# Performance work log

Hardware: AMD Instinct MI355X
Metric: run time of the kernel (lower is better)

Reference implementation:

```python
import jax, jax.numpy as jnp
import numpy as np

P = 9  # patch_size


def setup_inputs() -> dict:
    key = jax.random.key(0)
    k1, k2, k3, k4 = jax.random.split(key, 4)
    B, Cin, D, H, W = 1, 128, 36, 72, 72
    Cout = 128
    L = (D // P) * ((H * W) // P)  # 2304 non-overlapping patches
    x = jax.random.normal(k1, (B, Cin, D, H, W), dtype=jnp.float32)
    attentions = jax.random.normal(k2, (B, Cout, L, P * P), dtype=jnp.float32)
    Wc = jax.random.normal(k3, (Cout, Cin), dtype=jnp.float32) * 0.05  # conv_img 1x1x1 weight
    b = jax.random.normal(k4, (Cout,), dtype=jnp.float32) * 0.05
    return {"x": x, "attentions": attentions, "W": Wc, "b": b}


def reference(x, attentions, W, b):
    # conv_img: 1x1x1 Conv3d == per-voxel channel GEMM
    y = jnp.einsum('oc,bcdhw->bodhw', W, x) + b[None, :, None, None, None]
    B, C, D, H, Wd = y.shape
    HW = H * Wd
    y2 = y.reshape(1, C, D, HW)  # [1, C, D, H*W] as in the torch reshape
    nD, nW = D // P, HW // P
    # Unfold with kernel=stride=P (non-overlapping) == block reshape.
    # Column order: patches row-major; row order: kernel positions row-major.
    patches = (y2.reshape(1, C, nD, P, nW, P)
                 .transpose(0, 1, 2, 4, 3, 5)
                 .reshape(1, C, nD * nW, P * P))  # [1, C, L, P*P]
    nz = jnp.count_nonzero(attentions, axis=-1).astype(y2.dtype)[..., None] + 1e-5
    att = patches + attentions / nz  # [1, C, L, P*P]
    # Fold (non-overlapping) == inverse block reshape; no overlap accumulation.
    corr = (att.reshape(1, C, nD, nW, P, P)
               .transpose(0, 1, 2, 4, 3, 5)
               .reshape(1, C, D, HW))
    out = corr * y2 + y2
    return jnp.where(out >= 0, out, 0.2 * out)  # LeakyReLU(0.2)
```

## Files before the change

kernel.cpp:

```cpp
#include <hip/hip_runtime.h>

#define CIN   128
#define COUT  128
#define DD    36
#define HW    5184
#define DHW   186624
#define PATCH 9
#define NPW   576
#define L_TOT 2304
#define PP    81
#define LDSK  136

typedef __attribute__((ext_vector_type(8))) short bf16x8;
typedef __attribute__((ext_vector_type(4))) float f32x4;

__device__ __forceinline__ short f2bf(float f) {
    unsigned u = __builtin_bit_cast(unsigned, f);
    unsigned r = (u + 0x7fffu + ((u >> 16) & 1u)) >> 16;
    return (short)r;
}
__device__ __forceinline__ float bf2f(short s) {
    return __builtin_bit_cast(float, ((unsigned)(unsigned short)s) << 16);
}

__global__ __launch_bounds__(256) void count_ballot(
    const float* __restrict__ attn, float* __restrict__ inv)
{
    const int wv   = threadIdx.x >> 6;
    const int lane = threadIdx.x & 63;
    const int w    = blockIdx.x * 4 + wv;

    const unsigned long long P0X = (1ull << 21) - 1;
    const unsigned long long P0Y = (1ull << 20) - 1;
    const unsigned long long P1X = ((1ull << 20) - 1) << 21;
    const unsigned long long P1Y = ((1ull << 21) - 1) << 20;
    const unsigned long long P1Z = ((1ull << 20) - 1) << 20;
    const unsigned long long P2X = ((1ull << 20) - 1) << 41;
    const unsigned long long P2Z = ((1ull << 21) - 1) << 40;
    const unsigned long long P2W = ((1ull << 20) - 1) << 40;
    const unsigned long long P3X = 0x7ull << 61;
    const unsigned long long P3W = 0xFull << 60;
    const unsigned long long TL  = (1ull << 17) - 1;

    #pragma unroll
    for (int k = 0; k < 4; ++k) {
        const int g = w * 4 + k;
        const float4* ap = (const float4*)attn + (size_t)g * 81;
        const float4 va = ap[lane];
        float4 vb = (float4){0.f, 0.f, 0.f, 0.f};
        if (lane < 17) vb = ap[64 + lane];

        const unsigned long long bx = __ballot(va.x != 0.f);
        const unsigned long long by = __ballot(va.y != 0.f);
        const unsigned long long bz = __ballot(va.z != 0.f);
        const unsigned long long bw = __ballot(va.w != 0.f);
        const unsigned long long tx = __ballot(vb.x != 0.f);
        const unsigned long long ty = __ballot(vb.y != 0.f);
        const unsigned long long tz = __ballot(vb.z != 0.f);
        const unsigned long long tw = __ballot(vb.w != 0.f);

        const int c0 = __popcll(bx & P0X) + __popcll(by & P0Y)
                     + __popcll(bz & P0Y) + __popcll(bw & P0Y);
        const int c1 = __popcll(bx & P1X) + __popcll(by & P1Y)
                     + __popcll(bz & P1Z) + __popcll(bw & P1Z);
        const int c2 = __popcll(bx & P2X) + __popcll(by & P2X)
                     + __popcll(bz & P2Z) + __popcll(bw & P2W);
        const int c3 = __popcll(bx & P3X) + __popcll(by & P3X)
                     + __popcll(bz & P3X) + __popcll(bw & P3W)
                     + __popcll(tx & TL) + __popcll(ty & TL)
                     + __popcll(tz & TL) + __popcll(tw & TL);

        if (lane < 4) {
            const int cc = (lane == 0) ? c0 : (lane == 1) ? c1
                         : (lane == 2) ? c2 : c3;
            inv[(size_t)g * 4 + lane] = 1.0f / ((float)cc + 1e-5f);
        }
    }
}

__global__ __launch_bounds__(256, 4) void fused_main_v3(
    const float* __restrict__ x,
    const float* __restrict__ attn,
    const float* __restrict__ W,
    const float* __restrict__ bia,
    const float* __restrict__ inv,
    float* __restrict__ out)
{
    __shared__ __align__(16) short xs[64][LDSK];
    __shared__ short attn_s[128][76];
    __shared__ float inv_s[128][8];

    const int t    = threadIdx.x;
    const int wv   = t >> 6;
    const int lane = t & 63;
    const int col  = lane & 15;
    const int quad = lane >> 4;

    const int bidRaw = blockIdx.x;
    const int xcd = bidRaw & 7;
    const int loc = bidRaw >> 3;
    const int wgid = (xcd < 4 ? xcd * 365 : 1460 + (xcd - 4) * 364) + loc;

    const int d      = wgid % 36;
    const int hwblk  = wgid / 36;
    const int hwbase = hwblk * 64;
    const int lbase  = (d / 9) * NPW;
    const int ii     = d % 9;
    const int p0     = hwbase / 9;

    #pragma unroll
    for (int e = t; e < 1024; e += 256) {
        const int rp  = e >> 4;
        const int f4  = e & 15;
        const int row = rp * 2;
        const float* xp = x + (size_t)row * DHW + (size_t)d * HW + hwbase + f4 * 4;
        const float4 va = *(const float4*)xp;
        const float4 vb = *(const float4*)(xp + DHW);
        const int n0 = f4 * 4;
        const unsigned p0w = (unsigned short)f2bf(va.x) | ((unsigned)(unsigned short)f2bf(vb.x) << 16);
        const unsigned p1w = (unsigned short)f2bf(va.y) | ((unsigned)(unsigned short)f2bf(vb.y) << 16);
        const unsigned p2w = (unsigned short)f2bf(va.z) | ((unsigned)(unsigned short)f2bf(vb.z) << 16);
        const unsigned p3w = (unsigned short)f2bf(va.w) | ((unsigned)(unsigned short)f2bf(vb.w) << 16);
        *(unsigned*)&xs[n0 + 0][row] = p0w;
        *(unsigned*)&xs[n0 + 1][row] = p1w;
        *(unsigned*)&xs[n0 + 2][row] = p2w;
        *(unsigned*)&xs[n0 + 3][row] = p3w;
    }

    #pragma unroll
    for (int k = 0; k < 36; ++k) {
        const int e   = t + 256 * k;
        const int c   = e / 72;
        const int rem = e - c * 72;
        const int q   = rem / 9;
        const int j   = rem - q * 9;
        const float a = attn[(size_t)c * DHW + (size_t)(lbase + p0 + q) * PP
                             + ii * 9 + j];
        attn_s[c][rem] = f2bf(a);
    }
    #pragma unroll
    for (int k = 0; k < 4; ++k) {
        const int e = t + 256 * k;
        const int c = e >> 3, q = e & 7;
        inv_s[c][q] = inv[(size_t)c * L_TOT + lbase + p0 + q];
    }

    const int wbase = wv * 32;
    bf16x8 afrag[2][4];
    #pragma unroll
    for (int mt = 0; mt < 2; ++mt) {
        const int m = wbase + mt * 16 + col;
        #pragma unroll
        for (int s = 0; s < 4; ++s) {
            const float4* wp4 = (const float4*)(W + m * 128 + s * 32 + quad * 8);
            float4 w0 = wp4[0], w1 = wp4[1];
            bf16x8 f;
            f[0] = f2bf(w0.x); f[1] = f2bf(w0.y); f[2] = f2bf(w0.z); f[3] = f2bf(w0.w);
            f[4] = f2bf(w1.x); f[5] = f2bf(w1.y); f[6] = f2bf(w1.z); f[7] = f2bf(w1.w);
            afrag[mt][s] = f;
        }
    }
    float bias[2][4];
    #pragma unroll
    for (int mt = 0; mt < 2; ++mt)
        #pragma unroll
        for (int r = 0; r < 4; ++r)
            bias[mt][r] = bia[wbase + mt * 16 + quad * 4 + r];

    __syncthreads();

    f32x4 acc[2][4];
    #pragma unroll
    for (int mt = 0; mt < 2; ++mt)
        #pragma unroll
        for (int tt = 0; tt < 4; ++tt)
            acc[mt][tt] = (f32x4){0.f, 0.f, 0.f, 0.f};

    #pragma unroll
    for (int s = 0; s < 4; ++s) {
        bf16x8 bfrag[4];
        #pragma unroll
        for (int tt = 0; tt < 4; ++tt)
            bfrag[tt] = *(const bf16x8*)&xs[tt * 16 + col][s * 32 + quad * 8];
        #pragma unroll
        for (int mt = 0; mt < 2; ++mt)
            #pragma unroll
            for (int tt = 0; tt < 4; ++tt)
                acc[mt][tt] = __builtin_amdgcn_mfma_f32_16x16x32_bf16(
                    afrag[mt][s], bfrag[tt], acc[mt][tt], 0, 0, 0);
    }

    #pragma unroll
    for (int tt = 0; tt < 4; ++tt) {
        const int n  = tt * 16 + col;
        const int hw = hwbase + n;
        const int p  = hw / 9;
        const int jj = hw - p * 9;
        const int q  = p - p0;
        const int rem = q * 9 + jj;
        #pragma unroll
        for (int mt = 0; mt < 2; ++mt) {
            #pragma unroll
            for (int r = 0; r < 4; ++r) {
                const int c = wbase + mt * 16 + quad * 4 + r;
                const float y  = acc[mt][tt][r] + bias[mt][r];
                const float a  = bf2f(attn_s[c][rem]);
                const float iv = inv_s[c][q];
                const float v  = y * (y + a * iv + 1.0f);
                out[(size_t)c * DHW + (size_t)d * HW + hw] =
                    (v >= 0.f) ? v : 0.2f * v;
            }
        }
    }
}

__global__ __launch_bounds__(256) void fused_cross_head_fallback(
    const float* __restrict__ x, const float* __restrict__ attn,
    const float* __restrict__ W, const float* __restrict__ bia,
    float* __restrict__ out)
{
    __shared__ __align__(16) short xs[2][48][LDSK];
    __shared__ float inv_lds[COUT][4];

    const int t = threadIdx.x, wv = t >> 6, lane = t & 63;
    const int col = lane & 15, quad = lane >> 4;
    const int blk = blockIdx.x;
    const int pd = blk / 144, hwblk = blk - pd * 144;
    const int hwbase = hwblk * 36;
    const int lbase = pd * NPW + hwblk * 4;

    for (int pair = t; pair < 512; pair += 256) {
        const int c = pair >> 2, p = pair & 3;
        const float* ap = attn + (size_t)c * DHW + (size_t)(lbase + p) * PP;
        int cnt = 0;
        #pragma unroll 27
        for (int q = 0; q < PP; ++q) cnt += (ap[q] != 0.0f) ? 1 : 0;
        inv_lds[c][p] = 1.0f / ((float)cnt + 1e-5f);
    }
    const int wbase = wv * 32;
    bf16x8 afrag[2][4];
    #pragma unroll
    for (int mt = 0; mt < 2; ++mt) {
        const int m = wbase + mt * 16 + col;
        #pragma unroll
        for (int s = 0; s < 4; ++s) {
            const float4* wp4 = (const float4*)(W + m * 128 + s * 32 + quad * 8);
            float4 w0 = wp4[0], w1 = wp4[1];
            bf16x8 f;
            f[0] = f2bf(w0.x); f[1] = f2bf(w0.y); f[2] = f2bf(w0.z); f[3] = f2bf(w0.w);
            f[4] = f2bf(w1.x); f[5] = f2bf(w1.y); f[6] = f2bf(w1.z); f[7] = f2bf(w1.w);
            afrag[mt][s] = f;
        }
    }
    float bias[2][4];
    #pragma unroll
    for (int mt = 0; mt < 2; ++mt)
        #pragma unroll
        for (int r = 0; r < 4; ++r)
            bias[mt][r] = bia[wbase + mt * 16 + quad * 4 + r];

    for (int i = 0; i < 9; ++i) {
        const int buf = i & 1;
        const int d = pd * PATCH + i;
        for (int e = t; e < 1152; e += 256) {
            const int row = e / 9, f4 = e - row * 9;
            const float4 v = *(const float4*)(x + (size_t)row * DHW + (size_t)d * HW
                                              + hwbase + f4 * 4);
            const int n0 = f4 * 4;
            xs[buf][n0 + 0][row] = f2bf(v.x);
            xs[buf][n0 + 1][row] = f2bf(v.y);
            xs[buf][n0 + 2][row] = f2bf(v.z);
            xs[buf][n0 + 3][row] = f2bf(v.w);
        }
        __syncthreads();
        f32x4 acc[2][3];
        #pragma unroll
        for (int mt = 0; mt < 2; ++mt)
            #pragma unroll
            for (int tt = 0; tt < 3; ++tt)
                acc[mt][tt] = (f32x4){0.f, 0.f, 0.f, 0.f};
        #pragma unroll
        for (int s = 0; s < 4; ++s) {
            bf16x8 bfrag[3];
            #pragma unroll
            for (int tt = 0; tt < 3; ++tt)
                bfrag[tt] = *(const bf16x8*)&xs[buf][tt * 16 + col][s * 32 + quad * 8];
            #pragma unroll
            for (int mt = 0; mt < 2; ++mt)
                #pragma unroll
                for (int tt = 0; tt < 3; ++tt)
                    acc[mt][tt] = __builtin_amdgcn_mfma_f32_16x16x32_bf16(
                        afrag[mt][s], bfrag[tt], acc[mt][tt], 0, 0, 0);
        }
        #pragma unroll
        for (int tt = 0; tt < 3; ++tt) {
            const int n = tt * 16 + col;
            if (n < 36) {
                const int p = n / 9, jj = n - p * 9, kk = i * 9 + jj;
                #pragma unroll
                for (int mt = 0; mt < 2; ++mt) {
                    #pragma unroll
                    for (int r = 0; r < 4; ++r) {
                        const int c = wbase + mt * 16 + quad * 4 + r;
                        const float y = acc[mt][tt][r] + bias[mt][r];
                        const float a = attn[(size_t)c * DHW + (size_t)(lbase + p) * PP + kk];
                        const float v = y * (y + a * inv_lds[c][p] + 1.0f);
                        out[(size_t)c * DHW + (size_t)d * HW + hwbase + n] =
                            (v >= 0.f) ? v : 0.2f * v;
                    }
                }
            }
        }
        __syncthreads();
    }
}

extern "C" void kernel_launch(void* const* d_in, const int* in_sizes, int n_in,
                              void* d_out, int out_size, void* d_ws, size_t ws_size,
                              hipStream_t stream) {
    const float* x    = (const float*)d_in[0];
    const float* attn = (const float*)d_in[1];
    const float* W    = (const float*)d_in[2];
    const float* b    = (const float*)d_in[3];
    float* out        = (float*)d_out;

    const size_t inv_bytes = (size_t)COUT * L_TOT * sizeof(float);
    if (ws_size >= inv_bytes) {
        float* inv = (float*)d_ws;
        count_ballot<<<dim3(4608), dim3(256), 0, stream>>>(attn, inv);
        fused_main_v3<<<dim3(36 * 81), dim3(256), 0, stream>>>(x, attn, W, b, inv, out);
    } else {
        fused_cross_head_fallback<<<dim3(576), dim3(256), 0, stream>>>(x, attn, W, b, out);
    }
}
```

Measured before the change: 290.2 us.

## Process three depth slices per block with double-buffered x staging

```diff
diff --git a/kernel.cpp b/kernel.cpp
--- a/kernel.cpp
+++ b/kernel.cpp
@@ -18,9 +18,6 @@
     unsigned u = __builtin_bit_cast(unsigned, f);
     unsigned r = (u + 0x7fffu + ((u >> 16) & 1u)) >> 16;
     return (short)r;
-}
-__device__ __forceinline__ float bf2f(short s) {
-    return __builtin_bit_cast(float, ((unsigned)(unsigned short)s) << 16);
 }
 
 __global__ __launch_bounds__(256) void count_ballot(
@@ -78,7 +75,7 @@
     }
 }
 
-__global__ __launch_bounds__(256, 4) void fused_main_v3(
+__global__ __launch_bounds__(256, 4) void fused_pipe(
     const float* __restrict__ x,
     const float* __restrict__ attn,
     const float* __restrict__ W,
@@ -86,8 +83,7 @@
     const float* __restrict__ inv,
     float* __restrict__ out)
 {
-    __shared__ __align__(16) short xs[64][LDSK];
-    __shared__ short attn_s[128][76];
+    __shared__ __align__(16) short xs[2][64][LDSK];
     __shared__ float inv_s[128][8];
 
     const int t    = threadIdx.x;
@@ -96,55 +92,49 @@
     const int col  = lane & 15;
     const int quad = lane >> 4;
 
-    const int bidRaw = blockIdx.x;
-    const int xcd = bidRaw & 7;
-    const int loc = bidRaw >> 3;
-    const int wgid = (xcd < 4 ? xcd * 365 : 1460 + (xcd - 4) * 364) + loc;
-
-    const int d      = wgid % 36;
-    const int hwblk  = wgid / 36;
+    const int b      = blockIdx.x;
+    const int w0     = b * 3;
+    const int hwblk  = w0 / 36;
+    const int d0     = w0 - hwblk * 36;
     const int hwbase = hwblk * 64;
-    const int lbase  = (d / 9) * NPW;
-    const int ii     = d % 9;
+    const int pd     = d0 / 9;
+    const int lbase  = pd * NPW;
+    const int ii0    = d0 - pd * 9;
     const int p0     = hwbase / 9;
 
     #pragma unroll
-    for (int e = t; e < 1024; e += 256) {
-        const int rp  = e >> 4;
-        const int f4  = e & 15;
-        const int row = rp * 2;
-        const float* xp = x + (size_t)row * DHW + (size_t)d * HW + hwbase + f4 * 4;
-        const float4 va = *(const float4*)xp;
-        const float4 vb = *(const float4*)(xp + DHW);
-        const int n0 = f4 * 4;
-        const unsigned p0w = (unsigned short)f2bf(va.x) | ((unsigned)(unsigned short)f2bf(vb.x) << 16);
-        const unsigned p1w = (unsigned short)f2bf(va.y) | ((unsigned)(unsigned short)f2bf(vb.y) << 16);
-        const unsigned p2w = (unsigned short)f2bf(va.z) | ((unsigned)(unsigned short)f2bf(vb.z) << 16);
-        const unsigned p3w = (unsigned short)f2bf(va.w) | ((unsigned)(unsigned short)f2bf(vb.w) << 16);
-        *(unsigned*)&xs[n0 + 0][row] = p0w;
-        *(unsigned*)&xs[n0 + 1][row] = p1w;
-        *(unsigned*)&xs[n0 + 2][row] = p2w;
-        *(unsigned*)&xs[n0 + 3][row] = p3w;
-    }
-
-    #pragma unroll
-    for (int k = 0; k < 36; ++k) {
-        const int e   = t + 256 * k;
-        const int c   = e / 72;
-        const int rem = e - c * 72;
-        const int q   = rem / 9;
-        const int j   = rem - q * 9;
-        const float a = attn[(size_t)c * DHW + (size_t)(lbase + p0 + q) * PP
-                             + ii * 9 + j];
-        attn_s[c][rem] = f2bf(a);
-    }
-    #pragma unroll
-    for (int k = 0; k < 4; ++k) {
-        const int e = t + 256 * k;
+    for (int kk = 0; kk < 4; ++kk) {
+        const int e = t + 256 * kk;
         const int c = e >> 3, q = e & 7;
         inv_s[c][q] = inv[(size_t)c * L_TOT + lbase + p0 + q];
     }
 
+    float4 pva[4], pvb[4];
+
+#define ISSUE(IT, D) { \
+        const int e_ = t + 256 * (IT); \
+        const int rp_ = e_ >> 4, f4_ = e_ & 15; \
+        const float* xp_ = x + (size_t)(rp_ * 2) * DHW + (size_t)(D) * HW \
+                         + hwbase + f4_ * 4; \
+        pva[IT] = *(const float4*)xp_; \
+        pvb[IT] = *(const float4*)(xp_ + DHW); }
+
+#define WRITE(IT, BUF) { \
+        const int e_ = t + 256 * (IT); \
+        const int rp_ = e_ >> 4, f4_ = e_ & 15; \
+        const int row_ = rp_ * 2, n0_ = f4_ * 4; \
+        const float4 va_ = pva[IT], vb_ = pvb[IT]; \
+        *(unsigned*)&xs[BUF][n0_ + 0][row_] = \
+            (unsigned)(unsigned short)f2bf(va_.x) | ((unsigned)(unsigned short)f2bf(vb_.x) << 16); \
+        *(unsigned*)&xs[BUF][n0_ + 1][row_] = \
+            (unsigned)(unsigned short)f2bf(va_.y) | ((unsigned)(unsigned short)f2bf(vb_.y) << 16); \
+        *(unsigned*)&xs[BUF][n0_ + 2][row_] = \
+            (unsigned)(unsigned short)f2bf(va_.z) | ((unsigned)(unsigned short)f2bf(vb_.z) << 16); \
+        *(unsigned*)&xs[BUF][n0_ + 3][row_] = \
+            (unsigned)(unsigned short)f2bf(va_.w) | ((unsigned)(unsigned short)f2bf(vb_.w) << 16); }
+
+    ISSUE(0, d0) ISSUE(1, d0) ISSUE(2, d0) ISSUE(3, d0)
+
     const int wbase = wv * 32;
     bf16x8 afrag[2][4];
     #pragma unroll
@@ -153,10 +143,10 @@
         #pragma unroll
         for (int s = 0; s < 4; ++s) {
             const float4* wp4 = (const float4*)(W + m * 128 + s * 32 + quad * 8);
-            float4 w0 = wp4[0], w1 = wp4[1];
+            float4 w0v = wp4[0], w1v = wp4[1];
             bf16x8 f;
-            f[0] = f2bf(w0.x); f[1] = f2bf(w0.y); f[2] = f2bf(w0.z); f[3] = f2bf(w0.w);
-            f[4] = f2bf(w1.x); f[5] = f2bf(w1.y); f[6] = f2bf(w1.z); f[7] = f2bf(w1.w);
+            f[0] = f2bf(w0v.x); f[1] = f2bf(w0v.y); f[2] = f2bf(w0v.z); f[3] = f2bf(w0v.w);
+            f[4] = f2bf(w1v.x); f[5] = f2bf(w1v.y); f[6] = f2bf(w1v.z); f[7] = f2bf(w1v.w);
             afrag[mt][s] = f;
         }
     }
@@ -167,51 +157,71 @@
         for (int r = 0; r < 4; ++r)
             bias[mt][r] = bia[wbase + mt * 16 + quad * 4 + r];
 
+    WRITE(0, 0) WRITE(1, 0) WRITE(2, 0) WRITE(3, 0)
     __syncthreads();
 
-    f32x4 acc[2][4];
-    #pragma unroll
-    for (int mt = 0; mt < 2; ++mt)
-        #pragma unroll
-        for (int tt = 0; tt < 4; ++tt)
-            acc[mt][tt] = (f32x4){0.f, 0.f, 0.f, 0.f};
-
-    #pragma unroll
-    for (int s = 0; s < 4; ++s) {
-        bf16x8 bfrag[4];
-        #pragma unroll
-        for (int tt = 0; tt < 4; ++tt)
-            bfrag[tt] = *(const bf16x8*)&xs[tt * 16 + col][s * 32 + quad * 8];
+    #pragma unroll
+    for (int k = 0; k < 3; ++k) {
+        const int cb = k & 1, nb = cb ^ 1;
+        const int d  = d0 + k;
+        const int ii = ii0 + k;
+
+        if (k < 2) { ISSUE(0, d + 1) ISSUE(1, d + 1) }
+
+        f32x4 acc[2][4];
         #pragma unroll
         for (int mt = 0; mt < 2; ++mt)
             #pragma unroll
             for (int tt = 0; tt < 4; ++tt)
-                acc[mt][tt] = __builtin_amdgcn_mfma_f32_16x16x32_bf16(
-                    afrag[mt][s], bfrag[tt], acc[mt][tt], 0, 0, 0);
-    }
-
-    #pragma unroll
-    for (int tt = 0; tt < 4; ++tt) {
-        const int n  = tt * 16 + col;
-        const int hw = hwbase + n;
-        const int p  = hw / 9;
-        const int jj = hw - p * 9;
-        const int q  = p - p0;
-        const int rem = q * 9 + jj;
-        #pragma unroll
-        for (int mt = 0; mt < 2; ++mt) {
-            #pragma unroll
-            for (int r = 0; r < 4; ++r) {
-                const int c = wbase + mt * 16 + quad * 4 + r;
-                const float y  = acc[mt][tt][r] + bias[mt][r];
-                const float a  = bf2f(attn_s[c][rem]);
-                const float iv = inv_s[c][q];
-                const float v  = y * (y + a * iv + 1.0f);
-                out[(size_t)c * DHW + (size_t)d * HW + hw] =
-                    (v >= 0.f) ? v : 0.2f * v;
+                acc[mt][tt] = (f32x4){0.f, 0.f, 0.f, 0.f};
+
+        #pragma unroll
+        for (int s = 0; s < 4; ++s) {
+            bf16x8 bfrag[4];
+            #pragma unroll
+            for (int tt = 0; tt < 4; ++tt)
+                bfrag[tt] = *(const bf16x8*)&xs[cb][tt * 16 + col][s * 32 + quad * 8];
+            #pragma unroll
+            for (int mt = 0; mt < 2; ++mt)
+                #pragma unroll
+                for (int tt = 0; tt < 4; ++tt)
+                    acc[mt][tt] = __builtin_amdgcn_mfma_f32_16x16x32_bf16(
+                        afrag[mt][s], bfrag[tt], acc[mt][tt], 0, 0, 0);
+        }
+
+        if (k < 2) { ISSUE(2, d + 1) ISSUE(3, d + 1) }
+
+        #pragma unroll
+        for (int tt = 0; tt < 4; ++tt) {
+            const int n  = tt * 16 + col;
+            const int hw = hwbase + n;
+            const int p  = hw / 9;
+            const int jj = hw - p * 9;
+            const int q  = p - p0;
+            const int l  = lbase + p;
+            const int kidx = ii * 9 + jj;
+            #pragma unroll
+            for (int mt = 0; mt < 2; ++mt) {
+                #pragma unroll
+                for (int r = 0; r < 4; ++r) {
+                    const int c = wbase + mt * 16 + quad * 4 + r;
+                    const float y  = acc[mt][tt][r] + bias[mt][r];
+                    const float a  = attn[(size_t)c * DHW + (size_t)l * PP + kidx];
+                    const float iv = inv_s[c][q];
+                    const float v  = y * (y + a * iv + 1.0f);
+                    out[(size_t)c * DHW + (size_t)d * HW + hw] =
+                        fmaxf(v, 0.2f * v);
+                }
             }
         }
-    }
+
+        if (k < 2) {
+            WRITE(0, nb) WRITE(1, nb) WRITE(2, nb) WRITE(3, nb)
+        }
+        __syncthreads();
+    }
+#undef ISSUE
+#undef WRITE
 }
 
 __global__ __launch_bounds__(256) void fused_cross_head_fallback(
@@ -328,7 +338,7 @@
     if (ws_size >= inv_bytes) {
         float* inv = (float*)d_ws;
         count_ballot<<<dim3(4608), dim3(256), 0, stream>>>(attn, inv);
-        fused_main_v3<<<dim3(36 * 81), dim3(256), 0, stream>>>(x, attn, W, b, inv, out);
+        fused_pipe<<<dim3(972), dim3(256), 0, stream>>>(x, attn, W, b, inv, out);
     } else {
         fused_cross_head_fallback<<<dim3(576), dim3(256), 0, stream>>>(x, attn, W, b, out);
     }
```

Result: slower. 329.7 us (+13.6%).

## Stage attention and inverse counts via direct global-to-LDS loads, prefetch x into registers

Applied to the files above, without the earlier changes.

```diff
diff --git a/kernel.cpp b/kernel.cpp
--- a/kernel.cpp
+++ b/kernel.cpp
@@ -19,8 +19,11 @@
     unsigned r = (u + 0x7fffu + ((u >> 16) & 1u)) >> 16;
     return (short)r;
 }
-__device__ __forceinline__ float bf2f(short s) {
-    return __builtin_bit_cast(float, ((unsigned)(unsigned short)s) << 16);
+
+__device__ __forceinline__ void gload_lds4(const float* g, float* l) {
+    __builtin_amdgcn_global_load_lds(
+        (const __attribute__((address_space(1))) void*)g,
+        (__attribute__((address_space(3))) void*)l, 4, 0, 0);
 }
 
 __global__ __launch_bounds__(256) void count_ballot(
@@ -78,7 +81,7 @@
     }
 }
 
-__global__ __launch_bounds__(256, 4) void fused_main_v3(
+__global__ __launch_bounds__(256, 2) void fused_main_v4(
     const float* __restrict__ x,
     const float* __restrict__ attn,
     const float* __restrict__ W,
@@ -87,8 +90,8 @@
     float* __restrict__ out)
 {
     __shared__ __align__(16) short xs[64][LDSK];
-    __shared__ short attn_s[128][76];
-    __shared__ float inv_s[128][8];
+    __shared__ float attn_f[9216];
+    __shared__ float inv_f[1024];
 
     const int t    = threadIdx.x;
     const int wv   = t >> 6;
@@ -107,42 +110,40 @@
     const int lbase  = (d / 9) * NPW;
     const int ii     = d % 9;
     const int p0     = hwbase / 9;
-
-    #pragma unroll
-    for (int e = t; e < 1024; e += 256) {
-        const int rp  = e >> 4;
-        const int f4  = e & 15;
-        const int row = rp * 2;
-        const float* xp = x + (size_t)row * DHW + (size_t)d * HW + hwbase + f4 * 4;
-        const float4 va = *(const float4*)xp;
-        const float4 vb = *(const float4*)(xp + DHW);
-        const int n0 = f4 * 4;
-        const unsigned p0w = (unsigned short)f2bf(va.x) | ((unsigned)(unsigned short)f2bf(vb.x) << 16);
-        const unsigned p1w = (unsigned short)f2bf(va.y) | ((unsigned)(unsigned short)f2bf(vb.y) << 16);
-        const unsigned p2w = (unsigned short)f2bf(va.z) | ((unsigned)(unsigned short)f2bf(vb.z) << 16);
-        const unsigned p3w = (unsigned short)f2bf(va.w) | ((unsigned)(unsigned short)f2bf(vb.w) << 16);
-        *(unsigned*)&xs[n0 + 0][row] = p0w;
-        *(unsigned*)&xs[n0 + 1][row] = p1w;
-        *(unsigned*)&xs[n0 + 2][row] = p2w;
-        *(unsigned*)&xs[n0 + 3][row] = p3w;
-    }
-
-    #pragma unroll
-    for (int k = 0; k < 36; ++k) {
-        const int e   = t + 256 * k;
-        const int c   = e / 72;
-        const int rem = e - c * 72;
-        const int q   = rem / 9;
-        const int j   = rem - q * 9;
-        const float a = attn[(size_t)c * DHW + (size_t)(lbase + p0 + q) * PP
-                             + ii * 9 + j];
-        attn_s[c][rem] = f2bf(a);
-    }
-    #pragma unroll
-    for (int k = 0; k < 4; ++k) {
-        const int e = t + 256 * k;
-        const int c = e >> 3, q = e & 7;
-        inv_s[c][q] = inv[(size_t)c * L_TOT + lbase + p0 + q];
+    const int lp0    = lbase + p0;
+    const int iioff  = ii * 9;
+
+    float4 pva[4], pvb[4];
+    #pragma unroll
+    for (int it = 0; it < 4; ++it) {
+        const int e  = t + 256 * it;
+        const int rp = e >> 4, f4 = e & 15;
+        const float* xp = x + (size_t)(rp * 2) * DHW + (size_t)d * HW
+                        + hwbase + f4 * 4;
+        pva[it] = *(const float4*)xp;
+        pvb[it] = *(const float4*)(xp + DHW);
+    }
+
+    {
+        const int wbE = wv * 64;
+        #pragma unroll
+        for (int k = 0; k < 36; ++k) {
+            const int e   = k * 256 + wbE + lane;
+            const int c   = e / 72;
+            const int rem = e - c * 72;
+            const int q   = rem / 9;
+            const int j   = rem - q * 9;
+            const float* g = attn + (size_t)c * DHW + (size_t)(lp0 + q) * PP
+                           + iioff + j;
+            gload_lds4(g, &attn_f[k * 256 + wbE]);
+        }
+        #pragma unroll
+        for (int k = 0; k < 4; ++k) {
+            const int e = k * 256 + wbE + lane;
+            const int c = e >> 3, q = e & 7;
+            const float* g = inv + (size_t)c * L_TOT + lp0 + q;
+            gload_lds4(g, &inv_f[k * 256 + wbE]);
+        }
     }
 
     const int wbase = wv * 32;
@@ -167,6 +168,22 @@
         for (int r = 0; r < 4; ++r)
             bias[mt][r] = bia[wbase + mt * 16 + quad * 4 + r];
 
+    #pragma unroll
+    for (int it = 0; it < 4; ++it) {
+        const int e  = t + 256 * it;
+        const int rp = e >> 4, f4 = e & 15;
+        const int row = rp * 2, n0 = f4 * 4;
+        const float4 va = pva[it], vb = pvb[it];
+        *(unsigned*)&xs[n0 + 0][row] =
+            (unsigned)(unsigned short)f2bf(va.x) | ((unsigned)(unsigned short)f2bf(vb.x) << 16);
+        *(unsigned*)&xs[n0 + 1][row] =
+            (unsigned)(unsigned short)f2bf(va.y) | ((unsigned)(unsigned short)f2bf(vb.y) << 16);
+        *(unsigned*)&xs[n0 + 2][row] =
+            (unsigned)(unsigned short)f2bf(va.z) | ((unsigned)(unsigned short)f2bf(vb.z) << 16);
+        *(unsigned*)&xs[n0 + 3][row] =
+            (unsigned)(unsigned short)f2bf(va.w) | ((unsigned)(unsigned short)f2bf(vb.w) << 16);
+    }
+
     __syncthreads();
 
     f32x4 acc[2][4];
@@ -204,8 +221,8 @@
             for (int r = 0; r < 4; ++r) {
                 const int c = wbase + mt * 16 + quad * 4 + r;
                 const float y  = acc[mt][tt][r] + bias[mt][r];
-                const float a  = bf2f(attn_s[c][rem]);
-                const float iv = inv_s[c][q];
+                const float a  = attn_f[c * 72 + rem];
+                const float iv = inv_f[c * 8 + q];
                 const float v  = y * (y + a * iv + 1.0f);
                 out[(size_t)c * DHW + (size_t)d * HW + hw] =
                     (v >= 0.f) ? v : 0.2f * v;
@@ -328,7 +345,7 @@
     if (ws_size >= inv_bytes) {
         float* inv = (float*)d_ws;
         count_ballot<<<dim3(4608), dim3(256), 0, stream>>>(attn, inv);
-        fused_main_v3<<<dim3(36 * 81), dim3(256), 0, stream>>>(x, attn, W, b, inv, out);
+        fused_main_v4<<<dim3(36 * 81), dim3(256), 0, stream>>>(x, attn, W, b, inv, out);
     } else {
         fused_cross_head_fallback<<<dim3(576), dim3(256), 0, stream>>>(x, attn, W, b, out);
     }
```

Measured after the change: 279.8 us. -3.6%, faster.
